# Optimization experiments

Measured on AMD Instinct MI355X. Metric: run time of the kernel, lower is better.

The kernel has to match this reference:

```python
import jax, jax.numpy as jnp
import numpy as np

B, S, H, E, I = 2, 2048, 1024, 8, 4096
NUM_SELECT = 2


def setup_inputs() -> dict:
    key = jax.random.key(0)
    ks = jax.random.split(key, 6)
    scale = 0.02
    x = jax.random.normal(ks[0], (B, S, H), dtype=jnp.float32)
    Wg = jax.random.normal(ks[1], (H, E), dtype=jnp.float32) * scale
    W1 = jax.random.normal(ks[2], (E, H, I), dtype=jnp.float32) * scale
    b1 = jnp.zeros((E, I), dtype=jnp.float32)
    W2 = jax.random.normal(ks[3], (E, I, H), dtype=jnp.float32) * scale
    b2 = jnp.zeros((E, H), dtype=jnp.float32)
    return {"x": x, "Wg": Wg, "W1": W1, "b1": b1, "W2": W2, "b2": b2}


def reference(x, Wg, W1, b1, W2, b2):
    b, s, h = x.shape
    e = Wg.shape[1]
    xf = x.reshape(-1, h)                       # [T, H], T = b*s
    T = xf.shape[0]

    logits = xf @ Wg                            # [T, E]
    probs = jax.nn.softmax(logits, axis=-1)
    topk_p, topk_i = jax.lax.top_k(probs, NUM_SELECT)   # [T, k]
    topk_p = topk_p / topk_p.sum(axis=-1, keepdims=True)

    # combine weight per (token, expert): w[t, e] = sum_k topk_p[t, k] * 1[topk_i[t, k] == e]
    # top_k indices within a row are distinct, so scatter-add is exact.
    w = jnp.zeros((T, e), dtype=xf.dtype).at[jnp.arange(T)[:, None], topk_i].add(topk_p)

    # Dense per-expert FFN, weighted combine (weight is 0 for unrouted tokens,
    # so math matches the masked gather/scatter loop of the original).
    out = jnp.zeros_like(xf)
    for ei in range(e):  # small fixed loop over experts
        hdn = jax.nn.silu(xf @ W1[ei] + b1[ei])          # [T, I]
        y = hdn @ W2[ei] + b2[ei]                        # [T, H]
        out = out + w[:, ei:ei + 1] * y
    return out.reshape(b, s, h)
```

## Files before the change

kernel.cpp:

```cpp
#include <hip/hip_runtime.h>
#include <cstdint>
#include <cstddef>

using u16 = unsigned short;
typedef __bf16 bf16x8 __attribute__((ext_vector_type(8)));
typedef float f32x4 __attribute__((ext_vector_type(4)));

#define T_TOK 4096
#define HDIM 1024
#define EXP 8
#define IDIM 4096
#define NROWS 8192
#define PAD_ROWS 8320
#define BM 128
#define BN 128
#define BK 64
#define MAX_TILES 72

__device__ __forceinline__ u16 f2bf(float f) {
  union { float f; uint32_t u; } v; v.f = f;
  uint32_t u = v.u;
  u += 0x7fffu + ((u >> 16) & 1u);
  return (u16)(u >> 16);
}

__device__ __forceinline__ void async_copy16(const u16* g, u16* s) {
  __builtin_amdgcn_global_load_lds((__attribute__((address_space(1))) void*)(void*)g,
                                   (__attribute__((address_space(3))) void*)s, 16, 0, 0);
}

__global__ __launch_bounds__(256) void gate_kernel(const float* __restrict__ x,
                                                   const float* __restrict__ Wg,
                                                   int* __restrict__ sel_e,
                                                   float* __restrict__ sel_w) {
  int lane = threadIdx.x & 63;
  int wave = threadIdx.x >> 6;
  int t = blockIdx.x * 4 + wave;
  const float* xr = x + (size_t)t * HDIM;
  float p[8];
#pragma unroll
  for (int e = 0; e < 8; ++e) p[e] = 0.f;
#pragma unroll
  for (int i = 0; i < 16; ++i) {
    int h = i * 64 + lane;
    float xv = xr[h];
    const float4* w4 = (const float4*)(Wg + h * 8);
    float4 a = w4[0], b = w4[1];
    p[0] += xv * a.x; p[1] += xv * a.y; p[2] += xv * a.z; p[3] += xv * a.w;
    p[4] += xv * b.x; p[5] += xv * b.y; p[6] += xv * b.z; p[7] += xv * b.w;
  }
#pragma unroll
  for (int e = 0; e < 8; ++e) {
#pragma unroll
    for (int off = 32; off > 0; off >>= 1) p[e] += __shfl_xor(p[e], off);
  }
  if (lane == 0) {
    int e0 = 0; float m0 = p[0];
#pragma unroll
    for (int e = 1; e < 8; ++e) { if (p[e] > m0) { m0 = p[e]; e0 = e; } }
    int e1 = -1; float m1 = -3.4e38f;
#pragma unroll
    for (int e = 0; e < 8; ++e) { if (e != e0 && p[e] > m1) { m1 = p[e]; e1 = e; } }
    float r = expf(m1 - m0);
    float w0 = 1.f / (1.f + r);
    float w1 = r / (1.f + r);
    sel_e[2 * t] = e0; sel_e[2 * t + 1] = e1;
    sel_w[2 * t] = w0; sel_w[2 * t + 1] = w1;
  }
}

__global__ void route_kernel(const int* __restrict__ sel_e, const float* __restrict__ sel_w,
                             int* __restrict__ row_token, float* __restrict__ row_weight,
                             int* __restrict__ tile_e, int* __restrict__ tile_m0,
                             int* __restrict__ tile_nrows, int* __restrict__ num_tiles) {
  __shared__ int cnt[EXP], off[EXP], cur[EXP];
  int tid = threadIdx.x;
  if (tid < EXP) { cnt[tid] = 0; cur[tid] = 0; }
  __syncthreads();
  for (int i = tid; i < NROWS; i += 256) atomicAdd(&cnt[sel_e[i]], 1);
  __syncthreads();
  if (tid == 0) {
    int running = 0, nt = 0;
    for (int e = 0; e < EXP; ++e) {
      off[e] = running;
      int c = cnt[e];
      int ntile = (c + BM - 1) / BM;
      for (int j = 0; j < ntile; ++j) {
        tile_e[nt] = e;
        tile_m0[nt] = running + j * BM;
        tile_nrows[nt] = min(BM, c - j * BM);
        ++nt;
      }
      running += c;
    }
    *num_tiles = nt;
  }
  __syncthreads();
  for (int i = tid; i < NROWS; i += 256) {
    int e = sel_e[i];
    int pos = off[e] + atomicAdd(&cur[e], 1);
    row_token[pos] = i >> 1;
    row_weight[pos] = sel_w[i];
  }
}

__global__ __launch_bounds__(256) void gather_kernel(const float* __restrict__ x,
                                                     const int* __restrict__ row_token,
                                                     u16* __restrict__ xg) {
  int r = blockIdx.x;
  int tok = row_token[r];
  const float4* xs = (const float4*)(x + (size_t)tok * HDIM);
  float4 v = xs[threadIdx.x];
  ushort4 o;
  o.x = f2bf(v.x); o.y = f2bf(v.y); o.z = f2bf(v.z); o.w = f2bf(v.w);
  *(ushort4*)(xg + (size_t)r * HDIM + threadIdx.x * 4) = o;
}

__global__ __launch_bounds__(256) void transpose_convert(const float* __restrict__ src,
                                                         u16* __restrict__ dst, int R, int C) {
  int eb = blockIdx.z;
  const float* s = src + (size_t)eb * R * C;
  u16* d = dst + (size_t)eb * R * C;
  int cb = blockIdx.x * 64, rb = blockIdx.y * 64;
  __shared__ u16 tile[64][72];
  int tid = threadIdx.x;
#pragma unroll
  for (int i = 0; i < 4; ++i) {
    int idx = i * 256 + tid;
    int r = idx >> 4;
    int cq = (idx & 15) * 4;
    float4 v = *(const float4*)(s + (size_t)(rb + r) * C + cb + cq);
    tile[r][cq]     = f2bf(v.x);
    tile[r][cq + 1] = f2bf(v.y);
    tile[r][cq + 2] = f2bf(v.z);
    tile[r][cq + 3] = f2bf(v.w);
  }
  __syncthreads();
#pragma unroll
  for (int i = 0; i < 4; ++i) {
    int idx = i * 256 + tid;
    int c = idx >> 4;
    int rq = (idx & 15) * 4;
    ushort4 o;
    o.x = tile[rq][c]; o.y = tile[rq + 1][c]; o.z = tile[rq + 2][c]; o.w = tile[rq + 3][c];
    *(ushort4*)(d + (size_t)(cb + c) * R + rb + rq) = o;
  }
}

template <int K, bool SECOND>
__global__ __launch_bounds__(256, 2) void ffn_gemm(
    const u16* __restrict__ A, const u16* __restrict__ B,
    const float* __restrict__ bias, u16* __restrict__ hdn_out,
    float* __restrict__ out, const int* __restrict__ row_token,
    const float* __restrict__ row_weight, const int* __restrict__ tile_e,
    const int* __restrict__ tile_m0, const int* __restrict__ tile_nrows,
    const int* __restrict__ num_tiles, int N) {
  int ty = blockIdx.y;
  if (ty >= *num_tiles) return;
  int e = tile_e[ty];
  int row0 = tile_m0[ty];
  int nrows = tile_nrows[ty];
  int n0 = blockIdx.x * BN;

  __shared__ u16 sA[BM * BK];
  __shared__ u16 sB[BN * BK];

  int tid = threadIdx.x;
  int lane = tid & 63;
  int wave = tid >> 6;
  int wm = wave >> 1, wn = wave & 1;
  int l15 = lane & 15, quad = lane >> 4;
  int r7 = l15 & 7;

  const u16* Ab = A + (size_t)row0 * K;
  const u16* Bb = B + (size_t)e * (size_t)N * K + (size_t)n0 * K;

  const u16* pA[4]; const u16* pB[4];
  u16* dA[4]; u16* dB[4];
#pragma unroll
  for (int i = 0; i < 4; ++i) {
    int c = i * 256 + tid;
    int row = c >> 3;
    int j = (c & 7) ^ (row & 7);
    pA[i] = Ab + (size_t)row * K + j * 8;
    pB[i] = Bb + (size_t)row * K + j * 8;
    dA[i] = sA + c * 8;
    dB[i] = sB + c * 8;
  }

  int abase[4], bbase[4];
#pragma unroll
  for (int i = 0; i < 4; ++i) {
    abase[i] = (wm * 64 + i * 16 + l15) * BK;
    bbase[i] = (wn * 64 + i * 16 + l15) * BK;
  }
  int jx[2];
#pragma unroll
  for (int ks = 0; ks < 2; ++ks) jx[ks] = ((ks * 4 + quad) ^ r7) * 8;

  f32x4 acc[4][4];
#pragma unroll
  for (int am = 0; am < 4; ++am)
#pragma unroll
    for (int an = 0; an < 4; ++an) acc[am][an] = (f32x4){0.f, 0.f, 0.f, 0.f};

  for (int k0 = 0; k0 < K; k0 += BK) {
#pragma unroll
    for (int i = 0; i < 4; ++i) {
      async_copy16(pA[i] + k0, dA[i]);
      async_copy16(pB[i] + k0, dB[i]);
    }
    __syncthreads();
#pragma unroll
    for (int ks = 0; ks < 2; ++ks) {
      bf16x8 af[4], bfr[4];
#pragma unroll
      for (int i = 0; i < 4; ++i) af[i] = *(const bf16x8*)(sA + abase[i] + jx[ks]);
#pragma unroll
      for (int i = 0; i < 4; ++i) bfr[i] = *(const bf16x8*)(sB + bbase[i] + jx[ks]);
#pragma unroll
      for (int am = 0; am < 4; ++am)
#pragma unroll
        for (int an = 0; an < 4; ++an)
          acc[am][an] = __builtin_amdgcn_mfma_f32_16x16x32_bf16(af[am], bfr[an],
                                                               acc[am][an], 0, 0, 0);
    }
    __syncthreads();
  }

  if (!SECOND) {
#pragma unroll
    for (int an = 0; an < 4; ++an) {
      int col = n0 + wn * 64 + an * 16 + l15;
      float bv = bias[e * N + col];
#pragma unroll
      for (int am = 0; am < 4; ++am) {
#pragma unroll
        for (int r = 0; r < 4; ++r) {
          int lr = wm * 64 + am * 16 + quad * 4 + r;
          if (lr < nrows) {
            float vv = acc[am][an][r] + bv;
            vv = vv / (1.f + __expf(-vv));
            hdn_out[(size_t)(row0 + lr) * N + col] = f2bf(vv);
          }
        }
      }
    }
  } else {
    float bv[4];
#pragma unroll
    for (int an = 0; an < 4; ++an) bv[an] = bias[e * N + n0 + wn * 64 + an * 16 + l15];
#pragma unroll
    for (int am = 0; am < 4; ++am) {
#pragma unroll
      for (int r = 0; r < 4; ++r) {
        int lr = wm * 64 + am * 16 + quad * 4 + r;
        if (lr < nrows) {
          int grow = row0 + lr;
          int tok = row_token[grow];
          float w = row_weight[grow];
          float* orow = out + (size_t)tok * N;
#pragma unroll
          for (int an = 0; an < 4; ++an) {
            int col = n0 + wn * 64 + an * 16 + l15;
            atomicAdd(orow + col, (acc[am][an][r] + bv[an]) * w);
          }
        }
      }
    }
  }
}

extern "C" void kernel_launch(void* const* d_in, const int* in_sizes, int n_in,
                              void* d_out, int out_size, void* d_ws, size_t ws_size,
                              hipStream_t stream) {
  const float* x  = (const float*)d_in[0];
  const float* Wg = (const float*)d_in[1];
  const float* W1 = (const float*)d_in[2];
  const float* b1 = (const float*)d_in[3];
  const float* W2 = (const float*)d_in[4];
  const float* b2 = (const float*)d_in[5];
  float* out = (float*)d_out;

  char* ws = (char*)d_ws;
  size_t off = 0;
  auto alloc = [&](size_t bytes) {
    void* p = ws + off;
    off += (bytes + 255) & ~(size_t)255;
    return p;
  };
  u16* W1T = (u16*)alloc((size_t)EXP * IDIM * HDIM * 2);
  u16* W2T = (u16*)alloc((size_t)EXP * IDIM * HDIM * 2);
  u16* xg  = (u16*)alloc((size_t)PAD_ROWS * HDIM * 2);
  u16* hdn = (u16*)alloc((size_t)PAD_ROWS * IDIM * 2);
  int*   sel_e      = (int*)alloc(NROWS * 4);
  float* sel_w      = (float*)alloc(NROWS * 4);
  int*   row_token  = (int*)alloc(NROWS * 4);
  float* row_weight = (float*)alloc(NROWS * 4);
  int* tile_e     = (int*)alloc(MAX_TILES * 4);
  int* tile_m0    = (int*)alloc(MAX_TILES * 4);
  int* tile_nrows = (int*)alloc(MAX_TILES * 4);
  int* num_tiles  = (int*)alloc(4);

  hipMemsetAsync(d_out, 0, (size_t)out_size * sizeof(float), stream);
  transpose_convert<<<dim3(IDIM / 64, HDIM / 64, EXP), 256, 0, stream>>>(W1, W1T, HDIM, IDIM);
  transpose_convert<<<dim3(HDIM / 64, IDIM / 64, EXP), 256, 0, stream>>>(W2, W2T, IDIM, HDIM);
  gate_kernel<<<T_TOK / 4, 256, 0, stream>>>(x, Wg, sel_e, sel_w);
  route_kernel<<<1, 256, 0, stream>>>(sel_e, sel_w, row_token, row_weight,
                                      tile_e, tile_m0, tile_nrows, num_tiles);
  gather_kernel<<<NROWS, 256, 0, stream>>>(x, row_token, xg);
  ffn_gemm<HDIM, false><<<dim3(IDIM / BN, MAX_TILES), 256, 0, stream>>>(
      xg, W1T, b1, hdn, nullptr, nullptr, nullptr,
      tile_e, tile_m0, tile_nrows, num_tiles, IDIM);
  ffn_gemm<IDIM, true><<<dim3(HDIM / BN, MAX_TILES), 256, 0, stream>>>(
      hdn, W2T, b2, nullptr, out, row_token, row_weight,
      tile_e, tile_m0, tile_nrows, num_tiles, HDIM);
}
```

Before: 604.0 us.

## Split-K the second FFN GEMM and widen transpose stores

Adds a split-K dimension to the grouped GEMM so the down-projection runs with two K halves in parallel. The halves accumulate through the existing atomic adds, with bias added only by the first. This raises the block count for the N=1024 GEMM, which has only 8 column tiles per routed tile, at the cost of twice the atomic traffic to the output. The weight transpose also switches to 8-element vector stores with a 65-column shared tile to change the bank pattern.

```diff
diff --git a/kernel.cpp b/kernel.cpp
--- a/kernel.cpp
+++ b/kernel.cpp
@@ -5,6 +5,7 @@
 using u16 = unsigned short;
 typedef __bf16 bf16x8 __attribute__((ext_vector_type(8)));
 typedef float f32x4 __attribute__((ext_vector_type(4)));
+typedef u16 u16x8 __attribute__((ext_vector_type(8)));
 
 #define T_TOK 4096
 #define HDIM 1024
@@ -122,28 +123,29 @@
   const float* s = src + (size_t)eb * R * C;
   u16* d = dst + (size_t)eb * R * C;
   int cb = blockIdx.x * 64, rb = blockIdx.y * 64;
-  __shared__ u16 tile[64][72];
+  __shared__ u16 tile[64][65];
   int tid = threadIdx.x;
 #pragma unroll
   for (int i = 0; i < 4; ++i) {
     int idx = i * 256 + tid;
     int r = idx >> 4;
-    int cq = (idx & 15) * 4;
-    float4 v = *(const float4*)(s + (size_t)(rb + r) * C + cb + cq);
-    tile[r][cq]     = f2bf(v.x);
-    tile[r][cq + 1] = f2bf(v.y);
-    tile[r][cq + 2] = f2bf(v.z);
-    tile[r][cq + 3] = f2bf(v.w);
+    int c4 = (idx & 15) * 4;
+    float4 v = *(const float4*)(s + (size_t)(rb + r) * C + cb + c4);
+    tile[r][c4]     = f2bf(v.x);
+    tile[r][c4 + 1] = f2bf(v.y);
+    tile[r][c4 + 2] = f2bf(v.z);
+    tile[r][c4 + 3] = f2bf(v.w);
   }
   __syncthreads();
 #pragma unroll
-  for (int i = 0; i < 4; ++i) {
+  for (int i = 0; i < 2; ++i) {
     int idx = i * 256 + tid;
-    int c = idx >> 4;
-    int rq = (idx & 15) * 4;
-    ushort4 o;
-    o.x = tile[rq][c]; o.y = tile[rq + 1][c]; o.z = tile[rq + 2][c]; o.w = tile[rq + 3][c];
-    *(ushort4*)(d + (size_t)(cb + c) * R + rb + rq) = o;
+    int c = idx >> 3;
+    int r8 = (idx & 7) * 8;
+    u16x8 o;
+#pragma unroll
+    for (int j = 0; j < 8; ++j) o[j] = tile[r8 + j][c];
+    *(u16x8*)(d + (size_t)(cb + c) * R + rb + r8) = o;
   }
 }
 
@@ -154,13 +156,15 @@
     float* __restrict__ out, const int* __restrict__ row_token,
     const float* __restrict__ row_weight, const int* __restrict__ tile_e,
     const int* __restrict__ tile_m0, const int* __restrict__ tile_nrows,
-    const int* __restrict__ num_tiles, int N) {
+    const int* __restrict__ num_tiles, int N, int kchunk) {
   int ty = blockIdx.y;
   if (ty >= *num_tiles) return;
   int e = tile_e[ty];
   int row0 = tile_m0[ty];
   int nrows = tile_nrows[ty];
   int n0 = blockIdx.x * BN;
+  int kz = blockIdx.z;
+  int kbase = kz * kchunk;
 
   __shared__ u16 sA[BM * BK];
   __shared__ u16 sB[BN * BK];
@@ -182,8 +186,8 @@
     int c = i * 256 + tid;
     int row = c >> 3;
     int j = (c & 7) ^ (row & 7);
-    pA[i] = Ab + (size_t)row * K + j * 8;
-    pB[i] = Bb + (size_t)row * K + j * 8;
+    pA[i] = Ab + (size_t)row * K + j * 8 + kbase;
+    pB[i] = Bb + (size_t)row * K + j * 8 + kbase;
     dA[i] = sA + c * 8;
     dB[i] = sB + c * 8;
   }
@@ -204,7 +208,7 @@
 #pragma unroll
     for (int an = 0; an < 4; ++an) acc[am][an] = (f32x4){0.f, 0.f, 0.f, 0.f};
 
-  for (int k0 = 0; k0 < K; k0 += BK) {
+  for (int k0 = 0; k0 < kchunk; k0 += BK) {
 #pragma unroll
     for (int i = 0; i < 4; ++i) {
       async_copy16(pA[i] + k0, dA[i]);
@@ -249,7 +253,8 @@
   } else {
     float bv[4];
 #pragma unroll
-    for (int an = 0; an < 4; ++an) bv[an] = bias[e * N + n0 + wn * 64 + an * 16 + l15];
+    for (int an = 0; an < 4; ++an)
+      bv[an] = (kz == 0) ? bias[e * N + n0 + wn * 64 + an * 16 + l15] : 0.f;
 #pragma unroll
     for (int am = 0; am < 4; ++am) {
 #pragma unroll
@@ -309,10 +314,10 @@
   route_kernel<<<1, 256, 0, stream>>>(sel_e, sel_w, row_token, row_weight,
                                       tile_e, tile_m0, tile_nrows, num_tiles);
   gather_kernel<<<NROWS, 256, 0, stream>>>(x, row_token, xg);
-  ffn_gemm<HDIM, false><<<dim3(IDIM / BN, MAX_TILES), 256, 0, stream>>>(
+  ffn_gemm<HDIM, false><<<dim3(IDIM / BN, MAX_TILES, 1), 256, 0, stream>>>(
       xg, W1T, b1, hdn, nullptr, nullptr, nullptr,
-      tile_e, tile_m0, tile_nrows, num_tiles, IDIM);
-  ffn_gemm<IDIM, true><<<dim3(HDIM / BN, MAX_TILES), 256, 0, stream>>>(
+      tile_e, tile_m0, tile_nrows, num_tiles, IDIM, HDIM);
+  ffn_gemm<IDIM, true><<<dim3(HDIM / BN, MAX_TILES, 2), 256, 0, stream>>>(
       hdn, W2T, b2, nullptr, out, row_token, row_weight,
-      tile_e, tile_m0, tile_nrows, num_tiles, HDIM);
-}
+      tile_e, tile_m0, tile_nrows, num_tiles, HDIM, IDIM / 2);
+}
```

Result: slower. 622.9 us (+3.1%).
